# Kernel tuning notes

Measured on AMD Instinct MI355X. Metric: run time of the kernel, lower is better.

The kernel has to match this reference:

```python
import jax, jax.numpy as jnp
from jax import lax
import numpy as np
import math

# Static module config (matches init_kwargs)
K = 5            # kernel_size
MD = 3           # max_degree
HH = (MD + 1) ** 2   # n_harmonics = 16
CIN, F = 16, 32
B, D = 1, 48
NJ = K // 2      # n_radial_profiles (one shell per integer radius 1..K//2)
DN = ('NCDHW', 'OIDHW', 'NCDHW')


def _sh_table(ct, st, phi):
    """Complex spherical harmonics Y_n^m up to degree 3 (Condon-Shortley), [*grid, HH]."""
    fourpi = 4.0 * np.pi
    def N(n, m):
        return np.sqrt((2 * n + 1) / fourpi * math.factorial(n - m) / math.factorial(n + m))
    P = {
        (0, 0): np.ones_like(ct),
        (1, 0): ct,
        (1, 1): -st,
        (2, 0): 0.5 * (3 * ct ** 2 - 1),
        (2, 1): -3.0 * ct * st,
        (2, 2): 3.0 * st ** 2,
        (3, 0): 0.5 * (5 * ct ** 3 - 3 * ct),
        (3, 1): -1.5 * (5 * ct ** 2 - 1) * st,
        (3, 2): 15.0 * ct * st ** 2,
        (3, 3): -15.0 * st ** 3,
    }
    sh = np.zeros(ct.shape + (HH,), dtype=np.complex64)
    for n in range(MD + 1):
        for m in range(0, n + 1):
            y = (N(n, m) * P[(n, m)]).astype(np.complex64) * np.exp(1j * m * phi).astype(np.complex64)
            sh[..., n * n + n + m] = y
            if m > 0:
                sh[..., n * n + n - m] = ((-1) ** m) * np.conj(y)
    return sh


def _make_atoms():
    """Radial-shell x SH atoms: [K,K,K,NJ,HH] complex, L2-normalized per atom."""
    g = np.linspace(-(K // 2), K // 2, K)
    x, y, z = np.meshgrid(g, g, g, indexing='xy')
    r = np.sqrt(x * x + y * y + z * z)
    phi = np.arctan2(y, x)
    ct = np.divide(z, r, out=np.zeros_like(r), where=r != 0)
    st = np.sqrt(np.clip(1.0 - ct * ct, 0.0, None))
    sh = _sh_table(ct, st, phi)                                     # [K,K,K,HH]
    prof = np.stack([np.clip(1.0 - np.abs(r - j), 0.0, None) for j in range(1, NJ + 1)], -1)  # [K,K,K,NJ]
    atoms = prof[..., :, None] * sh[..., None, :]                   # [K,K,K,NJ,HH]
    norm = np.sqrt((np.abs(atoms) ** 2).sum(axis=(0, 1, 2), keepdims=True))
    atoms = atoms / np.where(norm > 0, norm, 1.0)
    return atoms.real.astype(np.float32), atoms.imag.astype(np.float32)


ATOMS_R, ATOMS_I = _make_atoms()
DEG = np.repeat(np.arange(MD + 1), 2 * np.arange(MD + 1) + 1)       # harmonic index -> degree (len HH)


def setup_inputs() -> dict:
    key = jax.random.key(0)
    ks = jax.random.split(key, 4)
    lim = float(np.sqrt(6.0 / (CIN + F)))
    return {
        'x': jax.random.normal(ks[0], (B, CIN, D, D, D), jnp.float32),
        'w': jax.random.uniform(ks[1], (CIN, F, NJ, MD + 1), jnp.float32, -lim, lim),
        'central_w': jax.random.uniform(ks[2], (F, CIN, 1, 1, 1), jnp.float32, -lim, lim),
        'central_b': jnp.zeros((F,), jnp.float32),
        'spec_bias': jnp.zeros(((MD + 1) * F,), jnp.float32),
        'proj_w': jax.random.uniform(ks[3], (F, (MD + 1) * F, 1, 1, 1), jnp.float32, -0.1, 0.1),
        'proj_b': jnp.zeros((F,), jnp.float32),
    }


def _forward(x, w, central_w, central_b, spec_bias, proj_w, proj_b):
    # Expand per-degree weights to per-harmonic (repeat_interleave over 2n+1 orders),
    # then fuse the per-channel SH conv + channel/radial weighted sum into a single
    # dense conv with composed kernels (same math as the torch loop + sum over axes 4,6).
    wh = w[..., DEG]                                                 # [C,F,NJ,HH]
    kr = jnp.einsum('cfjh,xyzjh->fhcxyz', wh, jnp.asarray(ATOMS_R)).reshape(F * HH, CIN, K, K, K)
    ki = jnp.einsum('cfjh,xyzjh->fhcxyz', wh, jnp.asarray(ATOMS_I)).reshape(F * HH, CIN, K, K, K)
    yr = lax.conv_general_dilated(x, kr, (1, 1, 1), 'SAME', dimension_numbers=DN)
    yi = lax.conv_general_dilated(x, ki, (1, 1, 1), 'SAME', dimension_numbers=DN)
    b, _, d, h, wd = yr.shape
    yr = yr.reshape(b, F, HH, d, h, wd)
    yi = yi.reshape(b, F, HH, d, h, wd)
    # 1x1x1 central-pixel conv added to the degree-0 (harmonic 0) real map
    cp = lax.conv_general_dilated(x, central_w, (1, 1, 1), 'SAME', dimension_numbers=DN)
    cp = cp + central_b[None, :, None, None, None]
    yr = yr.at[:, :, 0].add(cp)
    # rotation-invariant power spectrum per degree: 1/(2n+1) * sum_m (re^2 + im^2)
    p = yr * yr + yi * yi                                            # [B,F,HH,d,h,w]
    spec = jnp.stack([p[:, :, n * n:n * n + 2 * n + 1].sum(2) / (2 * n + 1) for n in range(MD + 1)], 2)
    spec = spec.reshape(b, F * (MD + 1), d, h, wd) + spec_bias[None, :, None, None, None]
    # activation=('Linear',...) is identity; projection 1x1x1 conv + ReLU
    out = lax.conv_general_dilated(spec, proj_w, (1, 1, 1), 'SAME', dimension_numbers=DN)
    out = out + proj_b[None, :, None, None, None]
    return jax.nn.relu(out)


def reference(x, w, central_w, central_b, spec_bias, proj_w, proj_b):
    return _forward(x, w, central_w, central_b, spec_bias, proj_w, proj_b)
```

## Files before the change

kernel.cpp:

```cpp
#include <hip/hip_runtime.h>
#include <hip/hip_fp16.h>
#include <math.h>


#define TX 8
#define TY 4
#define TZ 4
#define LXX 12
#define LYY 8
#define LZZ 8
#define NPOS 768
#define CPAD 24
#define POSB 48

#define ATAB2_B 0
#define WT2_B   23552
#define CW2_B   31744
#define PWT_B   32768
#define OB_B    49152
#define ED_B    49280

typedef __half2 h2;
union I4H { int4 v; h2 h[4]; };

__global__ __launch_bounds__(256) void ssh_init(
    const float* __restrict__ w, const float* __restrict__ cw,
    const float* __restrict__ proj_w, const float* __restrict__ spec_bias,
    const float* __restrict__ proj_b, char* __restrict__ wsb)
{
    __shared__ float shr[125][16];
    __shared__ float shi[125][16];
    __shared__ float prof[125][2];
    __shared__ float norms[2][16];
    __shared__ int epos[92];
    const int tid = threadIdx.x;
    const float fourpi = 4.0f * 3.14159265358979323846f;

    for (int p = tid; p < 125; p += 256) {
        int d2 = p % 5, d1 = (p / 5) % 5, d0 = p / 25;
        float xc = (float)(d1 - 2), yc = (float)(d0 - 2), zc = (float)(d2 - 2);
        float r2 = xc*xc + yc*yc + zc*zc;
        float r  = sqrtf(r2);
        float phi = atan2f(yc, xc);
        float ct = (r > 0.f) ? (zc / r) : 0.f;
        float st = sqrtf(fmaxf(0.f, 1.f - ct*ct));
        float c1 = cosf(phi), s1 = sinf(phi);
        float c2 = c1*c1 - s1*s1, s2 = 2.f*s1*c1;
        float c3 = c2*c1 - s2*s1, s3 = s2*c1 + c2*s1;
        float P10 = ct,              P11 = -st;
        float P20 = 0.5f*(3.f*ct*ct - 1.f), P21 = -3.f*ct*st, P22 = 3.f*st*st;
        float P30 = 0.5f*(5.f*ct*ct*ct - 3.f*ct);
        float P31 = -1.5f*(5.f*ct*ct - 1.f)*st;
        float P32 = 15.f*ct*st*st;
        float P33 = -15.f*st*st*st;
        float N00 = sqrtf(1.f/fourpi);
        float N10 = sqrtf(3.f/fourpi);
        float N11 = sqrtf(3.f/fourpi * 0.5f);
        float N20 = sqrtf(5.f/fourpi);
        float N21 = sqrtf(5.f/fourpi / 6.f);
        float N22 = sqrtf(5.f/fourpi / 24.f);
        float N30 = sqrtf(7.f/fourpi);
        float N31 = sqrtf(7.f/fourpi / 12.f);
        float N32 = sqrtf(7.f/fourpi / 120.f);
        float N33 = sqrtf(7.f/fourpi / 720.f);
        float b;
        shr[p][0] = N00;               shi[p][0] = 0.f;
        shr[p][2] = N10*P10;           shi[p][2] = 0.f;
        b = N11*P11;
        shr[p][3] =  b*c1;             shi[p][3] =  b*s1;
        shr[p][1] = -b*c1;             shi[p][1] =  b*s1;
        shr[p][6] = N20*P20;           shi[p][6] = 0.f;
        b = N21*P21;
        shr[p][7] =  b*c1;             shi[p][7] =  b*s1;
        shr[p][5] = -b*c1;             shi[p][5] =  b*s1;
        b = N22*P22;
        shr[p][8] =  b*c2;             shi[p][8] =  b*s2;
        shr[p][4] =  b*c2;             shi[p][4] = -b*s2;
        shr[p][12] = N30*P30;          shi[p][12] = 0.f;
        b = N31*P31;
        shr[p][13] =  b*c1;            shi[p][13] =  b*s1;
        shr[p][11] = -b*c1;            shi[p][11] =  b*s1;
        b = N32*P32;
        shr[p][14] =  b*c2;            shi[p][14] =  b*s2;
        shr[p][10] =  b*c2;            shi[p][10] = -b*s2;
        b = N33*P33;
        shr[p][15] =  b*c3;            shi[p][15] =  b*s3;
        shr[p][9]  = -b*c3;            shi[p][9]  =  b*s3;
        prof[p][0] = fmaxf(0.f, 1.f - fabsf(r - 1.f));
        prof[p][1] = fmaxf(0.f, 1.f - fabsf(r - 2.f));
    }
    __syncthreads();

    if (tid < 32) {
        int j = tid >> 4, h = tid & 15;
        float acc = 0.f;
        for (int p = 0; p < 125; ++p) {
            float pr = prof[p][j];
            acc += pr*pr*(shr[p][h]*shr[p][h] + shi[p][h]*shi[p][h]);
        }
        float nn = sqrtf(acc);
        norms[j][h] = (nn > 0.f) ? nn : 1.f;
    }
    if (tid < 125) {
        int p = tid;
        int d2 = p % 5, d1 = (p / 5) % 5, d0 = p / 25;
        int ix = d1 - 2, iy = d0 - 2, iz = d2 - 2;
        int r2i = ix*ix + iy*iy + iz*iz;
        int cls = (r2i == 1) ? 0 : (r2i == 2 || r2i == 3) ? 1
                : (r2i == 4 || r2i == 5 || r2i == 6 || r2i == 8) ? 2 : -1;
        if (cls >= 0) {
            int rank = (cls == 0) ? 0 : (cls == 1) ? 6 : 26;
            for (int q = 0; q < p; ++q) {
                int e2 = q % 5, e1 = (q / 5) % 5, e0 = q / 25;
                int jx = e1 - 2, jy = e0 - 2, jz = e2 - 2;
                int s2i = jx*jx + jy*jy + jz*jz;
                int c2i = (s2i == 1) ? 0 : (s2i == 2 || s2i == 3) ? 1
                       : (s2i == 4 || s2i == 5 || s2i == 6 || s2i == 8) ? 2 : -1;
                rank += (c2i == cls) ? 1 : 0;
            }
            epos[rank] = p;
            ((int*)(wsb + ED_B))[rank] = (d0*(LYY*LXX) + d1*LXX + d2) * POSB;
        }
    }
    __syncthreads();

    h2* at2 = (h2*)(wsb + ATAB2_B);
    for (int t = tid; t < 92*16; t += 256) {
        int e = t >> 4, h = t & 15;
        int p = epos[e];
        float c0 = prof[p][0] / norms[0][h];
        float c1v = prof[p][1] / norms[1][h];
        at2[(h*92+e)*4 + 0] = __float2half2_rn(c0*shr[p][h]);
        at2[(h*92+e)*4 + 1] = __float2half2_rn(c0*shi[p][h]);
        at2[(h*92+e)*4 + 2] = __float2half2_rn(c1v*shr[p][h]);
        at2[(h*92+e)*4 + 3] = __float2half2_rn(c1v*shi[p][h]);
    }
    h2* wt2h = (h2*)(wsb + WT2_B);
    for (int t = tid; t < 2048; t += 256) {
        int n = t >> 9, f = (t >> 4) & 31, j = (t >> 3) & 1, cp = t & 7;
        float a = w[((2*cp*32 + f)*2 + j)*4 + n];
        float b = w[(((2*cp+1)*32 + f)*2 + j)*4 + n];
        wt2h[t] = __halves2half2(__float2half(a), __float2half(b));
    }
    h2* cw2h = (h2*)(wsb + CW2_B);
    for (int t = tid; t < 256; t += 256) {
        int f = t >> 3, cp = t & 7;
        cw2h[t] = __halves2half2(__float2half(cw[f*16 + 2*cp]),
                                 __float2half(cw[f*16 + 2*cp + 1]));
    }
    float* pwT = (float*)(wsb + PWT_B);
    for (int t = tid; t < 4096; t += 256) {
        int i = t >> 5, fo = t & 31;
        pwT[t] = proj_w[fo*128 + i];
    }
    if (tid < 32) {
        float acc = proj_b[tid];
        for (int i = 0; i < 128; ++i) acc += proj_w[tid*128 + i] * spec_bias[i];
        ((float*)(wsb + OB_B))[tid] = acc;
    }
}


__device__ __forceinline__ void conv2c(const __half* __restrict__ ldsh, int baseb,
    const int4* __restrict__ aA, const int4* __restrict__ aB,
    const int* __restrict__ ed, h2 (&zA)[4][8], h2 (&zB)[4][8])
{
#pragma unroll
    for (int r = 0; r < 4; ++r)
#pragma unroll
        for (int q = 0; q < 8; ++q) { zA[r][q] = __float2half2_rn(0.f); zB[r][q] = __float2half2_rn(0.f); }

#pragma unroll 3
    for (int e = 0; e < 6; ++e) {
        I4H ca, cb_, x0, x1;
        ca.v = aA[e]; cb_.v = aB[e];
        const int4* p = (const int4*)((const char*)ldsh + baseb + ed[e]);
        x0.v = p[0]; x1.v = p[1];
#pragma unroll
        for (int q = 0; q < 4; ++q) {
            zA[0][q]   = __hfma2(ca.h[0],  x0.h[q], zA[0][q]);
            zA[1][q]   = __hfma2(ca.h[1],  x0.h[q], zA[1][q]);
            zB[0][q]   = __hfma2(cb_.h[0], x0.h[q], zB[0][q]);
            zB[1][q]   = __hfma2(cb_.h[1], x0.h[q], zB[1][q]);
            zA[0][q+4] = __hfma2(ca.h[0],  x1.h[q], zA[0][q+4]);
            zA[1][q+4] = __hfma2(ca.h[1],  x1.h[q], zA[1][q+4]);
            zB[0][q+4] = __hfma2(cb_.h[0], x1.h[q], zB[0][q+4]);
            zB[1][q+4] = __hfma2(cb_.h[1], x1.h[q], zB[1][q+4]);
        }
    }
#pragma unroll 4
    for (int e = 6; e < 26; ++e) {
        I4H ca, cb_, x0, x1;
        ca.v = aA[e]; cb_.v = aB[e];
        const int4* p = (const int4*)((const char*)ldsh + baseb + ed[e]);
        x0.v = p[0]; x1.v = p[1];
#pragma unroll
        for (int q = 0; q < 4; ++q) {
            zA[0][q]   = __hfma2(ca.h[0],  x0.h[q], zA[0][q]);
            zA[1][q]   = __hfma2(ca.h[1],  x0.h[q], zA[1][q]);
            zA[2][q]   = __hfma2(ca.h[2],  x0.h[q], zA[2][q]);
            zA[3][q]   = __hfma2(ca.h[3],  x0.h[q], zA[3][q]);
            zB[0][q]   = __hfma2(cb_.h[0], x0.h[q], zB[0][q]);
            zB[1][q]   = __hfma2(cb_.h[1], x0.h[q], zB[1][q]);
            zB[2][q]   = __hfma2(cb_.h[2], x0.h[q], zB[2][q]);
            zB[3][q]   = __hfma2(cb_.h[3], x0.h[q], zB[3][q]);
            zA[0][q+4] = __hfma2(ca.h[0],  x1.h[q], zA[0][q+4]);
            zA[1][q+4] = __hfma2(ca.h[1],  x1.h[q], zA[1][q+4]);
            zA[2][q+4] = __hfma2(ca.h[2],  x1.h[q], zA[2][q+4]);
            zA[3][q+4] = __hfma2(ca.h[3],  x1.h[q], zA[3][q+4]);
            zB[0][q+4] = __hfma2(cb_.h[0], x1.h[q], zB[0][q+4]);
            zB[1][q+4] = __hfma2(cb_.h[1], x1.h[q], zB[1][q+4]);
            zB[2][q+4] = __hfma2(cb_.h[2], x1.h[q], zB[2][q+4]);
            zB[3][q+4] = __hfma2(cb_.h[3], x1.h[q], zB[3][q+4]);
        }
    }
#pragma unroll 3
    for (int e = 26; e < 92; ++e) {
        I4H ca, cb_, x0, x1;
        ca.v = aA[e]; cb_.v = aB[e];
        const int4* p = (const int4*)((const char*)ldsh + baseb + ed[e]);
        x0.v = p[0]; x1.v = p[1];
#pragma unroll
        for (int q = 0; q < 4; ++q) {
            zA[2][q]   = __hfma2(ca.h[2],  x0.h[q], zA[2][q]);
            zA[3][q]   = __hfma2(ca.h[3],  x0.h[q], zA[3][q]);
            zB[2][q]   = __hfma2(cb_.h[2], x0.h[q], zB[2][q]);
            zB[3][q]   = __hfma2(cb_.h[3], x0.h[q], zB[3][q]);
            zA[2][q+4] = __hfma2(ca.h[2],  x1.h[q], zA[2][q+4]);
            zA[3][q+4] = __hfma2(ca.h[3],  x1.h[q], zA[3][q+4]);
            zB[2][q+4] = __hfma2(cb_.h[2], x1.h[q], zB[2][q+4]);
            zB[3][q+4] = __hfma2(cb_.h[3], x1.h[q], zB[3][q+4]);
        }
    }
}

__device__ __forceinline__ void conv1c(const __half* __restrict__ ldsh, int baseb,
    const int4* __restrict__ aA, const int* __restrict__ ed, h2 (&zA)[4][8])
{
#pragma unroll
    for (int r = 0; r < 4; ++r)
#pragma unroll
        for (int q = 0; q < 8; ++q) zA[r][q] = __float2half2_rn(0.f);

#pragma unroll 3
    for (int e = 0; e < 6; ++e) {
        I4H ca, x0, x1;
        ca.v = aA[e];
        const int4* p = (const int4*)((const char*)ldsh + baseb + ed[e]);
        x0.v = p[0]; x1.v = p[1];
#pragma unroll
        for (int q = 0; q < 4; ++q) {
            zA[0][q]   = __hfma2(ca.h[0], x0.h[q], zA[0][q]);
            zA[1][q]   = __hfma2(ca.h[1], x0.h[q], zA[1][q]);
            zA[0][q+4] = __hfma2(ca.h[0], x1.h[q], zA[0][q+4]);
            zA[1][q+4] = __hfma2(ca.h[1], x1.h[q], zA[1][q+4]);
        }
    }
#pragma unroll 4
    for (int e = 6; e < 26; ++e) {
        I4H ca, x0, x1;
        ca.v = aA[e];
        const int4* p = (const int4*)((const char*)ldsh + baseb + ed[e]);
        x0.v = p[0]; x1.v = p[1];
#pragma unroll
        for (int q = 0; q < 4; ++q) {
            zA[0][q]   = __hfma2(ca.h[0], x0.h[q], zA[0][q]);
            zA[1][q]   = __hfma2(ca.h[1], x0.h[q], zA[1][q]);
            zA[2][q]   = __hfma2(ca.h[2], x0.h[q], zA[2][q]);
            zA[3][q]   = __hfma2(ca.h[3], x0.h[q], zA[3][q]);
            zA[0][q+4] = __hfma2(ca.h[0], x1.h[q], zA[0][q+4]);
            zA[1][q+4] = __hfma2(ca.h[1], x1.h[q], zA[1][q+4]);
            zA[2][q+4] = __hfma2(ca.h[2], x1.h[q], zA[2][q+4]);
            zA[3][q+4] = __hfma2(ca.h[3], x1.h[q], zA[3][q+4]);
        }
    }
#pragma unroll 3
    for (int e = 26; e < 92; ++e) {
        I4H ca, x0, x1;
        ca.v = aA[e];
        const int4* p = (const int4*)((const char*)ldsh + baseb + ed[e]);
        x0.v = p[0]; x1.v = p[1];
#pragma unroll
        for (int q = 0; q < 4; ++q) {
            zA[2][q]   = __hfma2(ca.h[2], x0.h[q], zA[2][q]);
            zA[3][q]   = __hfma2(ca.h[3], x0.h[q], zA[3][q]);
            zA[2][q+4] = __hfma2(ca.h[2], x1.h[q], zA[2][q+4]);
            zA[3][q+4] = __hfma2(ca.h[3], x1.h[q], zA[3][q+4]);
        }
    }
}

__device__ __forceinline__ void conv2r(const __half* __restrict__ ldsh, int baseb,
    const int4* __restrict__ aA, const int4* __restrict__ aB,
    const int* __restrict__ ed, h2 (&z)[4][8])
{
#pragma unroll
    for (int r = 0; r < 4; ++r)
#pragma unroll
        for (int q = 0; q < 8; ++q) z[r][q] = __float2half2_rn(0.f);

#pragma unroll 3
    for (int e = 0; e < 6; ++e) {
        I4H ca, cb_, x0, x1;
        ca.v = aA[e]; cb_.v = aB[e];
        const int4* p = (const int4*)((const char*)ldsh + baseb + ed[e]);
        x0.v = p[0]; x1.v = p[1];
#pragma unroll
        for (int q = 0; q < 4; ++q) {
            z[0][q]   = __hfma2(ca.h[0],  x0.h[q], z[0][q]);
            z[2][q]   = __hfma2(cb_.h[0], x0.h[q], z[2][q]);
            z[0][q+4] = __hfma2(ca.h[0],  x1.h[q], z[0][q+4]);
            z[2][q+4] = __hfma2(cb_.h[0], x1.h[q], z[2][q+4]);
        }
    }
#pragma unroll 4
    for (int e = 6; e < 26; ++e) {
        I4H ca, cb_, x0, x1;
        ca.v = aA[e]; cb_.v = aB[e];
        const int4* p = (const int4*)((const char*)ldsh + baseb + ed[e]);
        x0.v = p[0]; x1.v = p[1];
#pragma unroll
        for (int q = 0; q < 4; ++q) {
            z[0][q]   = __hfma2(ca.h[0],  x0.h[q], z[0][q]);
            z[1][q]   = __hfma2(ca.h[2],  x0.h[q], z[1][q]);
            z[2][q]   = __hfma2(cb_.h[0], x0.h[q], z[2][q]);
            z[3][q]   = __hfma2(cb_.h[2], x0.h[q], z[3][q]);
            z[0][q+4] = __hfma2(ca.h[0],  x1.h[q], z[0][q+4]);
            z[1][q+4] = __hfma2(ca.h[2],  x1.h[q], z[1][q+4]);
            z[2][q+4] = __hfma2(cb_.h[0], x1.h[q], z[2][q+4]);
            z[3][q+4] = __hfma2(cb_.h[2], x1.h[q], z[3][q+4]);
        }
    }
#pragma unroll 3
    for (int e = 26; e < 92; ++e) {
        I4H ca, cb_, x0, x1;
        ca.v = aA[e]; cb_.v = aB[e];
        const int4* p = (const int4*)((const char*)ldsh + baseb + ed[e]);
        x0.v = p[0]; x1.v = p[1];
#pragma unroll
        for (int q = 0; q < 4; ++q) {
            z[1][q]   = __hfma2(ca.h[2],  x0.h[q], z[1][q]);
            z[3][q]   = __hfma2(cb_.h[2], x0.h[q], z[3][q]);
            z[1][q+4] = __hfma2(ca.h[2],  x1.h[q], z[1][q+4]);
            z[3][q+4] = __hfma2(cb_.h[2], x1.h[q], z[3][q+4]);
        }
    }
}


#define CDEL (2*(LYY*LXX) + 2*LXX + 2)

template<int N>
__device__ __forceinline__ void mixc2(const h2 (&zA)[4][8], const h2 (&zB)[4][8],
    const int4* __restrict__ wt2n, const float* __restrict__ pwT, float2 (&outa)[16])
{
    const float W = 2.f / (float)(2*N + 1);
#pragma unroll 2
    for (int f = 0; f < 32; ++f) {
        I4H w00, w01, w10, w11;
        w00.v = wt2n[f*4+0]; w01.v = wt2n[f*4+1];
        w10.v = wt2n[f*4+2]; w11.v = wt2n[f*4+3];
        h2 yrA = __float2half2_rn(0.f), yiA = __float2half2_rn(0.f);
        h2 yrB = __float2half2_rn(0.f), yiB = __float2half2_rn(0.f);
#pragma unroll
        for (int q = 0; q < 4; ++q) {
            yrA = __hfma2(w00.h[q], zA[0][q],   yrA);
            yrA = __hfma2(w01.h[q], zA[0][q+4], yrA);
            yrA = __hfma2(w10.h[q], zA[2][q],   yrA);
            yrA = __hfma2(w11.h[q], zA[2][q+4], yrA);
            yiA = __hfma2(w00.h[q], zA[1][q],   yiA);
            yiA = __hfma2(w01.h[q], zA[1][q+4], yiA);
            yiA = __hfma2(w10.h[q], zA[3][q],   yiA);
            yiA = __hfma2(w11.h[q], zA[3][q+4], yiA);
            yrB = __hfma2(w00.h[q], zB[0][q],   yrB);
            yrB = __hfma2(w01.h[q], zB[0][q+4], yrB);
            yrB = __hfma2(w10.h[q], zB[2][q],   yrB);
            yrB = __hfma2(w11.h[q], zB[2][q+4], yrB);
            yiB = __hfma2(w00.h[q], zB[1][q],   yiB);
            yiB = __hfma2(w01.h[q], zB[1][q+4], yiB);
            yiB = __hfma2(w10.h[q], zB[3][q],   yiB);
            yiB = __hfma2(w11.h[q], zB[3][q+4], yiB);
        }
        float ra = __low2float(yrA) + __high2float(yrA);
        float ia = __low2float(yiA) + __high2float(yiA);
        float rb = __low2float(yrB) + __high2float(yrB);
        float ib = __low2float(yiB) + __high2float(yiB);
        float s = (ra*ra + ia*ia + rb*rb + ib*ib) * W;
        const float2* pw2 = (const float2*)(pwT + (f*4 + N)*32);
#pragma unroll
        for (int k = 0; k < 16; ++k) {
            float2 t = pw2[k];
            outa[k].x = fmaf(t.x, s, outa[k].x);
            outa[k].y = fmaf(t.y, s, outa[k].y);
        }
    }
}

template<int RR, int N>
__device__ __forceinline__ void mix_cr(const h2 (&zC)[4][8], const h2 (&zR)[4][8],
    const int4* __restrict__ wt2n, const float* __restrict__ pwT, float2 (&outa)[16])
{
    const float Wc = 2.f / (float)(2*N + 1);
    const float Wr = 1.f / (float)(2*N + 1);
#pragma unroll 2
    for (int f = 0; f < 32; ++f) {
        I4H w00, w01, w10, w11;
        w00.v = wt2n[f*4+0]; w01.v = wt2n[f*4+1];
        w10.v = wt2n[f*4+2]; w11.v = wt2n[f*4+3];
        h2 yr = __float2half2_rn(0.f), yi = __float2half2_rn(0.f);
        h2 yR = __float2half2_rn(0.f);
#pragma unroll
        for (int q = 0; q < 4; ++q) {
            yr = __hfma2(w00.h[q], zC[0][q],   yr);
            yr = __hfma2(w01.h[q], zC[0][q+4], yr);
            yr = __hfma2(w10.h[q], zC[2][q],   yr);
            yr = __hfma2(w11.h[q], zC[2][q+4], yr);
            yi = __hfma2(w00.h[q], zC[1][q],   yi);
            yi = __hfma2(w01.h[q], zC[1][q+4], yi);
            yi = __hfma2(w10.h[q], zC[3][q],   yi);
            yi = __hfma2(w11.h[q], zC[3][q+4], yi);
            yR = __hfma2(w00.h[q], zR[RR][q],     yR);
            yR = __hfma2(w01.h[q], zR[RR][q+4],   yR);
            yR = __hfma2(w10.h[q], zR[RR+1][q],   yR);
            yR = __hfma2(w11.h[q], zR[RR+1][q+4], yR);
        }
        float rc = __low2float(yr) + __high2float(yr);
        float ic = __low2float(yi) + __high2float(yi);
        float rr = __low2float(yR) + __high2float(yR);
        float s = (rc*rc + ic*ic) * Wc + rr*rr * Wr;
        const float2* pw2 = (const float2*)(pwT + (f*4 + N)*32);
#pragma unroll
        for (int k = 0; k < 16; ++k) {
            float2 t = pw2[k];
            outa[k].x = fmaf(t.x, s, outa[k].x);
            outa[k].y = fmaf(t.y, s, outa[k].y);
        }
    }
}

template<int R, int N, bool CENTRAL>
__device__ __forceinline__ void mixr(const h2 (&z)[4][8],
    const int4* __restrict__ wt2n, const int4* __restrict__ cw2,
    const float* __restrict__ cbp, const __half* __restrict__ ldsh, int baseb,
    const float* __restrict__ pwT, float2 (&outa)[16])
{
    const float W = 1.f / (float)(2*N + 1);
    h2 xc[8];
    if (CENTRAL) {
        const int4* pc = (const int4*)((const char*)ldsh + baseb + CDEL*POSB);
        I4H xc0, xc1; xc0.v = pc[0]; xc1.v = pc[1];
#pragma unroll
        for (int q = 0; q < 4; ++q) { xc[q] = xc0.h[q]; xc[q+4] = xc1.h[q]; }
    }
#pragma unroll 2
    for (int f = 0; f < 32; ++f) {
        I4H w00, w01, w10, w11;
        w00.v = wt2n[f*4+0]; w01.v = wt2n[f*4+1];
        w10.v = wt2n[f*4+2]; w11.v = wt2n[f*4+3];
        h2 yr = __float2half2_rn(0.f);
#pragma unroll
        for (int q = 0; q < 4; ++q) {
            yr = __hfma2(w00.h[q], z[R][q],     yr);
            yr = __hfma2(w01.h[q], z[R][q+4],   yr);
            yr = __hfma2(w10.h[q], z[R+1][q],   yr);
            yr = __hfma2(w11.h[q], z[R+1][q+4], yr);
        }
        float yrf = __low2float(yr) + __high2float(yr);
        if (CENTRAL) {
            I4H c0, c1; c0.v = cw2[f*2]; c1.v = cw2[f*2+1];
            h2 acc = __float2half2_rn(0.f);
#pragma unroll
            for (int q = 0; q < 4; ++q) {
                acc = __hfma2(c0.h[q], xc[q],   acc);
                acc = __hfma2(c1.h[q], xc[q+4], acc);
            }
            yrf += cbp[f] + __low2float(acc) + __high2float(acc);
        }
        float s = yrf*yrf * W;
        const float2* pw2 = (const float2*)(pwT + (f*4 + N)*32);
#pragma unroll
        for (int k = 0; k < 16; ++k) {
            float2 t = pw2[k];
            outa[k].x = fmaf(t.x, s, outa[k].x);
            outa[k].y = fmaf(t.y, s, outa[k].y);
        }
    }
}

__global__ __launch_bounds__(256, 3) void ssh_main(
    const float* __restrict__ x, const float* __restrict__ cb,
    const char* __restrict__ wsb, float* __restrict__ out)
{
    __shared__ __align__(16) __half ldsh[NPOS * CPAD];
    const int tid = threadIdx.x;
    const int x0 = blockIdx.x * TX, y0 = blockIdx.y * TY, z0 = blockIdx.z * TZ;

    for (int i = tid; i < NPOS * 8; i += 256) {
        int cp = i / NPOS;
        int pos = i - cp * NPOS;
        int lx = pos % LXX; int t1 = pos / LXX;
        int ly = t1 % LYY;  int lz = t1 / LYY;
        int gx = x0 + lx - 2, gy = y0 + ly - 2, gz = z0 + lz - 2;
        h2 hv = __float2half2_rn(0.f);
        if ((unsigned)gx < 48u && (unsigned)gy < 48u && (unsigned)gz < 48u) {
            int gi = ((2*cp*48 + gz)*48 + gy)*48 + gx;
            hv = __floats2half2_rn(x[gi], x[gi + 48*48*48]);
        }
        *(h2*)(ldsh + pos*CPAD + 2*cp) = hv;
    }
    __syncthreads();

    const int hf  = tid >> 7;
    const int vid = tid & 127;
    const int tx = vid & 7, ty = (vid >> 3) & 3, tz = vid >> 5;
    const int baseb = (tz*(LYY*LXX) + ty*LXX + tx) * POSB;

    const int4* __restrict__ atab = (const int4*)(wsb + ATAB2_B);
    const int*  __restrict__ ed   = (const int*)(wsb + ED_B);
    const int4* __restrict__ wt2  = (const int4*)(wsb + WT2_B);
    const int4* __restrict__ cw2  = (const int4*)(wsb + CW2_B);
    const float* __restrict__ pwT = (const float*)(wsb + PWT_B);
    const float* __restrict__ obase = (const float*)(wsb + OB_B);

    float2 outa[16];
#pragma unroll
    for (int k = 0; k < 16; ++k) outa[k] = make_float2(0.f, 0.f);

    h2 zA[4][8], zB[4][8];
    if (hf == 0) {
        conv2c(ldsh, baseb, atab + 13*92, atab + 14*92, ed, zA, zB);
        mixc2<3>(zA, zB, wt2 + 3*128, pwT, outa);
        conv1c(ldsh, baseb, atab + 15*92, ed, zA);
        conv2r(ldsh, baseb, atab + 12*92, atab + 0*92, ed, zB);
        mix_cr<0,3>(zA, zB, wt2 + 3*128, pwT, outa);
        mixr<2,0,true>(zB, wt2 + 0*128, cw2, cb, ldsh, baseb, pwT, outa);
    } else {
        conv2c(ldsh, baseb, atab + 7*92, atab + 8*92, ed, zA, zB);
        mixc2<2>(zA, zB, wt2 + 2*128, pwT, outa);
        conv2r(ldsh, baseb, atab + 6*92, atab + 2*92, ed, zA);
        conv1c(ldsh, baseb, atab + 3*92, ed, zB);
        mix_cr<2,1>(zB, zA, wt2 + 1*128, pwT, outa);
        mixr<0,2,false>(zA, wt2 + 2*128, cw2, cb, ldsh, baseb, pwT, outa);
    }

    __syncthreads();
    float* lmerge = (float*)ldsh;
    if (hf == 1) {
#pragma unroll
        for (int k = 0; k < 16; ++k) {
            lmerge[vid*33 + 2*k]     = outa[k].x;
            lmerge[vid*33 + 2*k + 1] = outa[k].y;
        }
    }
    __syncthreads();
    if (hf == 0) {
        const int gz = z0 + tz, gy = y0 + ty, gx = x0 + tx;
#pragma unroll
        for (int k = 0; k < 16; ++k) {
            float v0 = obase[2*k]   + outa[k].x + lmerge[vid*33 + 2*k];
            float v1 = obase[2*k+1] + outa[k].y + lmerge[vid*33 + 2*k + 1];
            out[(((2*k)*48   + gz)*48 + gy)*48 + gx] = fmaxf(v0, 0.f);
            out[(((2*k+1)*48 + gz)*48 + gy)*48 + gx] = fmaxf(v1, 0.f);
        }
    }
}

extern "C" void kernel_launch(void* const* d_in, const int* in_sizes, int n_in,
                              void* d_out, int out_size, void* d_ws, size_t ws_size,
                              hipStream_t stream) {
    const float* x  = (const float*)d_in[0];
    const float* w  = (const float*)d_in[1];
    const float* cw = (const float*)d_in[2];
    const float* cb = (const float*)d_in[3];
    const float* sb = (const float*)d_in[4];
    const float* pw = (const float*)d_in[5];
    const float* pb = (const float*)d_in[6];
    float* out = (float*)d_out;
    char* wsb = (char*)d_ws;

    ssh_init<<<dim3(1), dim3(256), 0, stream>>>(w, cw, pw, sb, pb, wsb);
    ssh_main<<<dim3(48/TX, 48/TY, 48/TZ), dim3(256), 0, stream>>>(x, cb, wsb, out);
}
```

Measured before the change: 160.3 us.

## Split per-block harmonic work across four thread groups with 512-thread blocks

The kernel doubles the block to 512 threads and splits the two per-group conv/mix chains into four groups of 128 threads, so each thread runs roughly half the serial work. Partial projection outputs are combined through a two-level LDS tree reduction, which adds one extra barrier and a second merge buffer. The intent is more waves in flight and shorter per-thread critical paths. The launch bound is tightened to (512, 6), which could force a much smaller register budget and cause spilling of the large zA/zB/outa register arrays.

```diff
diff --git a/kernel.cpp b/kernel.cpp
--- a/kernel.cpp
+++ b/kernel.cpp
@@ -487,7 +487,7 @@
     }
 }
 
-__global__ __launch_bounds__(256, 3) void ssh_main(
+__global__ __launch_bounds__(512, 6) void ssh_main(
     const float* __restrict__ x, const float* __restrict__ cb,
     const char* __restrict__ wsb, float* __restrict__ out)
 {
@@ -495,7 +495,7 @@
     const int tid = threadIdx.x;
     const int x0 = blockIdx.x * TX, y0 = blockIdx.y * TY, z0 = blockIdx.z * TZ;
 
-    for (int i = tid; i < NPOS * 8; i += 256) {
+    for (int i = tid; i < NPOS * 8; i += 512) {
         int cp = i / NPOS;
         int pos = i - cp * NPOS;
         int lx = pos % LXX; int t1 = pos / LXX;
@@ -510,7 +510,7 @@
     }
     __syncthreads();
 
-    const int hf  = tid >> 7;
+    const int hg  = tid >> 7;
     const int vid = tid & 127;
     const int tx = vid & 7, ty = (vid >> 3) & 3, tz = vid >> 5;
     const int baseb = (tz*(LYY*LXX) + ty*LXX + tx) * POSB;
@@ -527,16 +527,18 @@
     for (int k = 0; k < 16; ++k) outa[k] = make_float2(0.f, 0.f);
 
     h2 zA[4][8], zB[4][8];
-    if (hf == 0) {
+    if (hg == 0) {
         conv2c(ldsh, baseb, atab + 13*92, atab + 14*92, ed, zA, zB);
         mixc2<3>(zA, zB, wt2 + 3*128, pwT, outa);
+    } else if (hg == 1) {
         conv1c(ldsh, baseb, atab + 15*92, ed, zA);
         conv2r(ldsh, baseb, atab + 12*92, atab + 0*92, ed, zB);
         mix_cr<0,3>(zA, zB, wt2 + 3*128, pwT, outa);
         mixr<2,0,true>(zB, wt2 + 0*128, cw2, cb, ldsh, baseb, pwT, outa);
-    } else {
+    } else if (hg == 2) {
         conv2c(ldsh, baseb, atab + 7*92, atab + 8*92, ed, zA, zB);
         mixc2<2>(zA, zB, wt2 + 2*128, pwT, outa);
+    } else {
         conv2r(ldsh, baseb, atab + 6*92, atab + 2*92, ed, zA);
         conv1c(ldsh, baseb, atab + 3*92, ed, zB);
         mix_cr<2,1>(zB, zA, wt2 + 1*128, pwT, outa);
@@ -545,20 +547,45 @@
 
     __syncthreads();
     float* lmerge = (float*)ldsh;
-    if (hf == 1) {
+    if (hg == 1) {
 #pragma unroll
         for (int k = 0; k < 16; ++k) {
             lmerge[vid*33 + 2*k]     = outa[k].x;
             lmerge[vid*33 + 2*k + 1] = outa[k].y;
         }
+    } else if (hg == 3) {
+#pragma unroll
+        for (int k = 0; k < 16; ++k) {
+            lmerge[4224 + vid*33 + 2*k]     = outa[k].x;
+            lmerge[4224 + vid*33 + 2*k + 1] = outa[k].y;
+        }
     }
     __syncthreads();
-    if (hf == 0) {
+    if (hg == 0) {
+#pragma unroll
+        for (int k = 0; k < 16; ++k) {
+            outa[k].x += lmerge[vid*33 + 2*k];
+            outa[k].y += lmerge[vid*33 + 2*k + 1];
+        }
+    } else if (hg == 2) {
+#pragma unroll
+        for (int k = 0; k < 16; ++k) {
+            outa[k].x += lmerge[4224 + vid*33 + 2*k];
+            outa[k].y += lmerge[4224 + vid*33 + 2*k + 1];
+        }
+#pragma unroll
+        for (int k = 0; k < 16; ++k) {
+            lmerge[4224 + vid*33 + 2*k]     = outa[k].x;
+            lmerge[4224 + vid*33 + 2*k + 1] = outa[k].y;
+        }
+    }
+    __syncthreads();
+    if (hg == 0) {
         const int gz = z0 + tz, gy = y0 + ty, gx = x0 + tx;
 #pragma unroll
         for (int k = 0; k < 16; ++k) {
-            float v0 = obase[2*k]   + outa[k].x + lmerge[vid*33 + 2*k];
-            float v1 = obase[2*k+1] + outa[k].y + lmerge[vid*33 + 2*k + 1];
+            float v0 = obase[2*k]   + outa[k].x + lmerge[4224 + vid*33 + 2*k];
+            float v1 = obase[2*k+1] + outa[k].y + lmerge[4224 + vid*33 + 2*k + 1];
             out[(((2*k)*48   + gz)*48 + gy)*48 + gx] = fmaxf(v0, 0.f);
             out[(((2*k+1)*48 + gz)*48 + gy)*48 + gx] = fmaxf(v1, 0.f);
         }
@@ -579,5 +606,5 @@
     char* wsb = (char*)d_ws;
 
     ssh_init<<<dim3(1), dim3(256), 0, stream>>>(w, cw, pw, sb, pb, wsb);
-    ssh_main<<<dim3(48/TX, 48/TY, 48/TZ), dim3(256), 0, stream>>>(x, cb, wsb, out);
-}
+    ssh_main<<<dim3(48/TX, 48/TY, 48/TZ), dim3(512), 0, stream>>>(x, cb, wsb, out);
+}
```

After: 422.2 us. +163.4%, slower.
